# Optimization experiments

Hardware: AMD Instinct MI355X
Metric: run time of the kernel (lower is better)

Reference implementation:

```python
import jax, jax.numpy as jnp
import numpy as np

B, L, DIM, N_STATE, K_CONV = 2, 2048, 1024, 16, 4


def setup_inputs() -> dict:
    key = jax.random.key(0)
    ks = jax.random.split(key, 6)
    sc = lambda k, shape, s: jax.random.normal(k, shape, jnp.float32) * s
    return {
        "x": jax.random.normal(ks[0], (B, L, DIM), jnp.float32),
        "in_proj_w": sc(ks[1], (2 * DIM, DIM), 0.02),
        "conv_w": sc(ks[2], (DIM, 1, K_CONV), 0.1),
        "conv_b": jnp.zeros((DIM,), jnp.float32),
        "x_proj_w": sc(ks[3], (2 * N_STATE + DIM, DIM), 0.02),
        "D_param": jnp.ones((DIM,), jnp.float32),
        "out_proj_w": sc(ks[4], (DIM, DIM), 0.02),
    }


def reference(x, in_proj_w, conv_w, conv_b, x_proj_w, D_param, out_proj_w):
    b, l, d = x.shape
    n = (x_proj_w.shape[0] - d) // 2
    k = conv_w.shape[-1]
    # A buffer: -[1..n] broadcast over channels -> [d, n]
    A = -(jnp.arange(1, n + 1, dtype=x.dtype)[None, :] * jnp.ones((d, 1), x.dtype))

    xz = x @ in_proj_w.T                       # [b, l, 2d]
    x_c, z = xz[..., :d], xz[..., d:]

    # depthwise causal conv (torch pads both sides k-1 then truncates to l == left-pad k-1)
    xc = jnp.transpose(x_c, (0, 2, 1))          # [b, d, l]
    xc = jax.lax.conv_general_dilated(
        xc, conv_w, window_strides=(1,), padding=[(k - 1, 0)],
        dimension_numbers=("NCH", "OIH", "NCH"), feature_group_count=d)
    xc = xc + conv_b[None, :, None]
    xc = jax.nn.silu(jnp.transpose(xc, (0, 2, 1)))  # [b, l, d]

    x_dbl = xc @ x_proj_w.T                    # [b, l, 2n + d]
    B_ssm = x_dbl[..., :n]                     # [b, l, n]
    C_ssm = x_dbl[..., n:2 * n]                # [b, l, n]
    dt = jax.nn.softplus(x_dbl[..., 2 * n:])   # [b, l, d]

    dA = jnp.exp(dt[..., None] * A[None, None])            # [b, l, d, n]
    dBx = (dt[..., None] * B_ssm[:, :, None, :]) * xc[..., None]  # dB * x, [b, l, d, n]

    def step(h, inputs):
        dA_t, dBx_t, C_t = inputs              # [b,d,n], [b,d,n], [b,n]
        h = h * dA_t + dBx_t
        y_t = jnp.einsum("bdn,bn->bd", h, C_t)
        return h, y_t

    h0 = jnp.zeros((b, d, n), x.dtype)
    _, ys = jax.lax.scan(
        step, h0,
        (jnp.moveaxis(dA, 1, 0), jnp.moveaxis(dBx, 1, 0), jnp.moveaxis(C_ssm, 1, 0)))
    y = jnp.moveaxis(ys, 0, 1) + D_param * xc  # [b, l, d]
    y = y * jax.nn.silu(z)
    return y @ out_proj_w.T
```

## Files before the change

kernel.cpp:

```cpp
#include <hip/hip_runtime.h>
#include <cmath>

#define BB   2
#define LL   2048
#define DIMD 1024
#define NS   16
#define KC   4
#define ML   (BB*LL)
#define XZ_N (2*DIMD)
#define XD_N (2*NS + DIMD)
#define LC   16
#define NC   (LL/LC)

typedef __attribute__((ext_vector_type(8))) short bf16x8;
typedef __attribute__((ext_vector_type(4))) float f32x4;

__device__ __forceinline__ unsigned short f2bf(float f) {
    union { float f; unsigned u; } v; v.f = f;
    unsigned r = v.u + 0x7FFF + ((v.u >> 16) & 1);
    return (unsigned short)(r >> 16);
}
__device__ __forceinline__ float bf2f(unsigned short u) {
    union { unsigned u; float f; } v; v.u = (unsigned)u << 16;
    return v.f;
}
__device__ __forceinline__ float silu_f(float a) {
    return a / (1.f + __expf(-a));
}
__device__ __forceinline__ void dt_decay(float raw, float& dt, float& e) {
    const float t = __expf(fminf(raw, 80.f));
    e  = 1.f / (1.f + t);
    dt = (raw > 15.f) ? raw : -__logf(e);
}

__global__ __launch_bounds__(256) void cvt_all(
    const float* __restrict__ s0, unsigned short* __restrict__ d0, int n0,
    const float* __restrict__ s1, unsigned short* __restrict__ d1, int n1,
    const float* __restrict__ s2, unsigned short* __restrict__ d2, int n2,
    const float* __restrict__ s3, unsigned short* __restrict__ d3, int n3)
{
    int i = blockIdx.x * blockDim.x + threadIdx.x;
    const float* src; unsigned short* dst;
    if (i < n0)                { src = s0; dst = d0; }
    else if ((i -= n0) < n1)   { src = s1; dst = d1; }
    else if ((i -= n1) < n2)   { src = s2; dst = d2; }
    else if ((i -= n2) < n3)   { src = s3; dst = d3; }
    else return;
    float4 f = ((const float4*)src)[i];
    ushort4 o;
    o.x = f2bf(f.x); o.y = f2bf(f.y); o.z = f2bf(f.z); o.w = f2bf(f.w);
    ((ushort4*)dst)[i] = o;
}

__global__ __launch_bounds__(256) void gemm_mfma_bt(
    const unsigned short* __restrict__ A,
    const unsigned short* __restrict__ Bw,
    float* __restrict__ C,
    unsigned short* __restrict__ zb,
    int M, int N, int K, int nsplit)
{
    __shared__ short As[2][128 * 64];
    __shared__ short Bs[2][64 * 64];

    const int nwg  = gridDim.x * gridDim.y;
    int wgid = blockIdx.y * gridDim.x + blockIdx.x;
    const int cpx = nwg >> 3;
    wgid = (wgid & 7) * cpx + (wgid >> 3);
    const int bx = wgid % gridDim.x;
    const int by = wgid / gridDim.x;

    const int tid  = threadIdx.x;
    const int lane = tid & 63;
    const int wave = tid >> 6;
    const int bm = by * 128;
    const int bn = bx * 64;
    const int wm = wave * 32;
    const int l15  = lane & 15;
    const int quad = lane >> 4;

    f32x4 acc[2][4];
    #pragma unroll
    for (int i = 0; i < 2; ++i)
        #pragma unroll
        for (int j = 0; j < 4; ++j)
            acc[i][j] = (f32x4){0.f, 0.f, 0.f, 0.f};

    const int NK = K >> 6;

    auto stage = [&](int s, int k0) {
        #pragma unroll
        for (int q = 0; q < 4; ++q) {
            const int ci = q * 256 + tid;
            const int r  = ci >> 3;
            const int cc = (ci & 7) ^ (r & 7);
            short* ldsA = &As[s][0] + (size_t)(q * 256 + (tid & ~63)) * 8;
            const unsigned short* ga = A + (size_t)(bm + r) * K + k0 + cc * 8;
            __builtin_amdgcn_global_load_lds(
                (const __attribute__((address_space(1))) void*)ga,
                (__attribute__((address_space(3))) void*)ldsA, 16, 0, 0);
        }
        #pragma unroll
        for (int q = 0; q < 2; ++q) {
            const int ci = q * 256 + tid;
            const int r  = ci >> 3;
            const int cc = (ci & 7) ^ (r & 7);
            short* ldsB = &Bs[s][0] + (size_t)(q * 256 + (tid & ~63)) * 8;
            int rb = bn + r; if (rb > N - 1) rb = N - 1;
            const unsigned short* gb = Bw + (size_t)rb * K + k0 + cc * 8;
            __builtin_amdgcn_global_load_lds(
                (const __attribute__((address_space(1))) void*)gb,
                (__attribute__((address_space(3))) void*)ldsB, 16, 0, 0);
        }
    };

    stage(0, 0);

    int cur = 0;
    for (int t = 0; t < NK; ++t) {
        if (t + 1 < NK) {
            stage(cur ^ 1, (t + 1) * 64);
            asm volatile("s_waitcnt vmcnt(6)" ::: "memory");
        } else {
            asm volatile("s_waitcnt vmcnt(0)" ::: "memory");
        }
        __builtin_amdgcn_s_barrier();

        const short* Ab = &As[cur][0];
        const short* Bb = &Bs[cur][0];
        #pragma unroll
        for (int kh = 0; kh < 2; ++kh) {
            bf16x8 af[2], bfr[4];
            #pragma unroll
            for (int i = 0; i < 2; ++i) {
                const int row = wm + i * 16 + l15;
                const int pc  = (kh * 4 + quad) ^ (row & 7);
                af[i] = *(const bf16x8*)(Ab + row * 64 + pc * 8);
            }
            #pragma unroll
            for (int j = 0; j < 4; ++j) {
                const int row = j * 16 + l15;
                const int pc  = (kh * 4 + quad) ^ (row & 7);
                bfr[j] = *(const bf16x8*)(Bb + row * 64 + pc * 8);
            }
            #pragma unroll
            for (int i = 0; i < 2; ++i)
                #pragma unroll
                for (int j = 0; j < 4; ++j)
                    acc[i][j] = __builtin_amdgcn_mfma_f32_16x16x32_bf16(
                        af[i], bfr[j], acc[i][j], 0, 0, 0);
        }

        if (t + 1 < NK) __builtin_amdgcn_s_barrier();
        cur ^= 1;
    }

    #pragma unroll
    for (int i = 0; i < 2; ++i) {
        const int rbase = bm + wm + i * 16 + quad * 4;
        #pragma unroll
        for (int j = 0; j < 4; ++j) {
            const int col = bn + j * 16 + l15;
            if (col < nsplit) {
                #pragma unroll
                for (int r = 0; r < 4; ++r)
                    C[(size_t)(rbase + r) * nsplit + col] = acc[i][j][r];
            } else if (col < N) {
                const int zc = col - nsplit;
                #pragma unroll
                for (int r = 0; r < 4; ++r)
                    zb[(size_t)(rbase + r) * DIMD + zc] = f2bf(silu_f(acc[i][j][r]));
            }
        }
    }
}

__global__ __launch_bounds__(256) void conv_silu(const float* __restrict__ xcraw,
                                                 const float* __restrict__ w,
                                                 const float* __restrict__ bias,
                                                 float* __restrict__ xc,
                                                 unsigned short* __restrict__ xcb)
{
    const int i4 = blockIdx.x * blockDim.x + threadIdx.x;
    if (i4 >= ML * DIMD / 4) return;
    const int dq = i4 & (DIMD / 4 - 1);
    const int bl = i4 >> 8;
    const int l  = bl & (LL - 1);

    const float4 wq0 = ((const float4*)w)[dq * 4 + 0];
    const float4 wq1 = ((const float4*)w)[dq * 4 + 1];
    const float4 wq2 = ((const float4*)w)[dq * 4 + 2];
    const float4 wq3 = ((const float4*)w)[dq * 4 + 3];
    const float4 bv  = ((const float4*)bias)[dq];

    const float* p = xcraw + (size_t)bl * DIMD + dq * 4;
    const float4 z4 = make_float4(0.f, 0.f, 0.f, 0.f);
    const float4 x0 = (l >= 3) ? *(const float4*)(p - 3 * DIMD) : z4;
    const float4 x1 = (l >= 2) ? *(const float4*)(p - 2 * DIMD) : z4;
    const float4 x2 = (l >= 1) ? *(const float4*)(p - 1 * DIMD) : z4;
    const float4 x3 = *(const float4*)p;

    float4 a;
    a.x = bv.x + wq0.x*x0.x + wq0.y*x1.x + wq0.z*x2.x + wq0.w*x3.x;
    a.y = bv.y + wq1.x*x0.y + wq1.y*x1.y + wq1.z*x2.y + wq1.w*x3.y;
    a.z = bv.z + wq2.x*x0.z + wq2.y*x1.z + wq2.z*x2.z + wq2.w*x3.z;
    a.w = bv.w + wq3.x*x0.w + wq3.y*x1.w + wq3.z*x2.w + wq3.w*x3.w;

    float4 v;
    v.x = silu_f(a.x); v.y = silu_f(a.y); v.z = silu_f(a.z); v.w = silu_f(a.w);

    ((float4*)xc)[i4] = v;
    ushort4 o;
    o.x = f2bf(v.x); o.y = f2bf(v.y); o.z = f2bf(v.z); o.w = f2bf(v.w);
    ((ushort4*)xcb)[i4] = o;
}

__global__ __launch_bounds__(256) void scan_part1(const float* __restrict__ xdbl,
                                                  const float* __restrict__ xc,
                                                  float* __restrict__ hfin,
                                                  float* __restrict__ Ssum)
{
    __shared__ float Bsh[LC][NS];

    const int tid = threadIdx.x;
    const int idx = blockIdx.x * 256 + tid;
    const int d   = idx & (DIMD - 1);
    const int bc  = idx >> 10;
    const int c   = bc & (NC - 1);
    const int b   = bc >> 7;
    const int l0  = c * LC;

    const float* xdbl_p = xdbl + ((size_t)b * LL + l0) * XD_N;
    const float* xc_p   = xc   + ((size_t)b * LL + l0) * DIMD + d;

    if (tid < LC * NS / 4) {
        const int l = tid >> 2, q = tid & 3;
        ((float4*)&Bsh[l][0])[q] = ((const float4*)(xdbl_p + (size_t)l * XD_N))[q];
    }
    __syncthreads();

    float raw[LC], xcv[LC];
    #pragma unroll
    for (int i = 0; i < LC; ++i) raw[i] = xdbl_p[(size_t)i * XD_N + 2 * NS + d];
    #pragma unroll
    for (int i = 0; i < LC; ++i) xcv[i] = xc_p[(size_t)i * DIMD];

    float e[LC], dx[LC];
    float S = 0.f;
    #pragma unroll
    for (int i = 0; i < LC; ++i) {
        float dt, ev;
        dt_decay(raw[i], dt, ev);
        S += dt;
        e[i]  = ev;
        dx[i] = dt * xcv[i];
    }

    float h[NS];
    #pragma unroll
    for (int n = 0; n < NS; ++n) h[n] = 0.f;

    #pragma unroll
    for (int i = 0; i < LC; ++i) {
        const float4* BC = (const float4*)&Bsh[i][0];
        const float4 B0 = BC[0], B1 = BC[1], B2 = BC[2], B3 = BC[3];
        const float ev = e[i], dxv = dx[i];
        const float e2 = ev * ev, e4 = e2 * e2;
        float p0 = ev, p1 = e2, p2 = e2 * ev, p3 = e4;
        h[0]  = fmaf(h[0],  p0, dxv * B0.x);
        h[1]  = fmaf(h[1],  p1, dxv * B0.y);
        h[2]  = fmaf(h[2],  p2, dxv * B0.z);
        h[3]  = fmaf(h[3],  p3, dxv * B0.w);
        p0 *= e4; p1 *= e4; p2 *= e4; p3 *= e4;
        h[4]  = fmaf(h[4],  p0, dxv * B1.x);
        h[5]  = fmaf(h[5],  p1, dxv * B1.y);
        h[6]  = fmaf(h[6],  p2, dxv * B1.z);
        h[7]  = fmaf(h[7],  p3, dxv * B1.w);
        p0 *= e4; p1 *= e4; p2 *= e4; p3 *= e4;
        h[8]  = fmaf(h[8],  p0, dxv * B2.x);
        h[9]  = fmaf(h[9],  p1, dxv * B2.y);
        h[10] = fmaf(h[10], p2, dxv * B2.z);
        h[11] = fmaf(h[11], p3, dxv * B2.w);
        p0 *= e4; p1 *= e4; p2 *= e4; p3 *= e4;
        h[12] = fmaf(h[12], p0, dxv * B3.x);
        h[13] = fmaf(h[13], p1, dxv * B3.y);
        h[14] = fmaf(h[14], p2, dxv * B3.z);
        h[15] = fmaf(h[15], p3, dxv * B3.w);
    }

    float4* hf = (float4*)(hfin + (size_t)idx * NS);
    #pragma unroll
    for (int n = 0; n < 4; ++n) hf[n] = ((float4*)h)[n];
    Ssum[idx] = S;
}

#define NGRP 8
#define CPG  (NC / NGRP)
__global__ __launch_bounds__(256) void scan_combine(float* __restrict__ hfin,
                                                    const float* __restrict__ Ssum)
{
    __shared__ float Ash[2][NGRP][NS];
    __shared__ float Bsh2[2][NGRP][NS];

    const int tid = threadIdx.x;
    const int n   = tid & (NS - 1);
    const int g   = (tid >> 4) & (NGRP - 1);
    const int d2  = tid >> 7;
    const int bd  = blockIdx.x * 2 + d2;
    const int d   = bd & (DIMD - 1);
    const int b   = bd >> 10;
    const float np1 = (float)(n + 1);
    const int c0 = g * CPG;

    float e[CPG], hb[CPG];
    #pragma unroll
    for (int j = 0; j < CPG; ++j) {
        const size_t base = ((size_t)(b * NC + c0 + j) * DIMD + d);
        const float S = Ssum[base];
        hb[j] = hfin[base * NS + n];
        e[j]  = __expf(-S * np1);
    }

    float A = 1.f, Bv = 0.f;
    #pragma unroll
    for (int j = 0; j < CPG; ++j) { Bv = fmaf(Bv, e[j], hb[j]); A *= e[j]; }

    Ash[d2][g][n] = A;  Bsh2[d2][g][n] = Bv;
    __syncthreads();

    float hc = 0.f;
    for (int j = 0; j < g; ++j) hc = fmaf(hc, Ash[d2][j][n], Bsh2[d2][j][n]);

    #pragma unroll
    for (int j = 0; j < CPG; ++j) {
        const size_t o = ((size_t)(b * NC + c0 + j) * DIMD + d) * NS + n;
        hfin[o] = hc;
        hc = fmaf(hc, e[j], hb[j]);
    }
}

__global__ __launch_bounds__(256) void scan_part2(const float* __restrict__ xdbl,
                                                  const float* __restrict__ xc,
                                                  const unsigned short* __restrict__ zb,
                                                  const float* __restrict__ hfin,
                                                  const float* __restrict__ Dp,
                                                  unsigned short* __restrict__ yout)
{
    __shared__ float BCs[LC][2 * NS];

    const int tid = threadIdx.x;
    const int idx = blockIdx.x * 256 + tid;
    const int d   = idx & (DIMD - 1);
    const int bc  = idx >> 10;
    const int c   = bc & (NC - 1);
    const int b   = bc >> 7;
    const int l0  = c * LC;

    const float* xdbl_p = xdbl + ((size_t)b * LL + l0) * XD_N;
    const float* xc_p   = xc   + ((size_t)b * LL + l0) * DIMD + d;
    const unsigned short* zb_p = zb + ((size_t)b * LL + l0) * DIMD + d;
    unsigned short* y_p = yout + ((size_t)b * LL + l0) * DIMD + d;

    if (tid < LC * 2 * NS / 4) {
        const int l = tid >> 3, q = tid & 7;
        ((float4*)&BCs[l][0])[q] = ((const float4*)(xdbl_p + (size_t)l * XD_N))[q];
    }
    __syncthreads();

    float raw[LC], xcv[LC], zg[LC];
    #pragma unroll
    for (int i = 0; i < LC; ++i) raw[i] = xdbl_p[(size_t)i * XD_N + 2 * NS + d];
    #pragma unroll
    for (int i = 0; i < LC; ++i) xcv[i] = xc_p[(size_t)i * DIMD];
    #pragma unroll
    for (int i = 0; i < LC; ++i) zg[i] = bf2f(zb_p[(size_t)i * DIMD]);

    float e[LC], dx[LC];
    #pragma unroll
    for (int i = 0; i < LC; ++i) {
        float dt, ev;
        dt_decay(raw[i], dt, ev);
        e[i]  = ev;
        dx[i] = dt * xcv[i];
    }

    const float Dv = Dp[d];
    float h[NS];
    {
        const float4* hf = (const float4*)(hfin + (size_t)idx * NS);
        #pragma unroll
        for (int n = 0; n < 4; ++n) ((float4*)h)[n] = hf[n];
    }

    #pragma unroll
    for (int i = 0; i < LC; ++i) {
        const float4* BC = (const float4*)&BCs[i][0];
        const float4 B0 = BC[0], B1 = BC[1], B2 = BC[2], B3 = BC[3];
        const float4 C0 = BC[4], C1 = BC[5], C2 = BC[6], C3 = BC[7];
        const float ev = e[i], dxv = dx[i];
        const float e2 = ev * ev, e4 = e2 * e2;
        float p0 = ev, p1 = e2, p2 = e2 * ev, p3 = e4;
        float y0, y1, y2, y3;
        h[0]  = fmaf(h[0],  p0, dxv * B0.x); y0 = h[0]  * C0.x;
        h[1]  = fmaf(h[1],  p1, dxv * B0.y); y1 = h[1]  * C0.y;
        h[2]  = fmaf(h[2],  p2, dxv * B0.z); y2 = h[2]  * C0.z;
        h[3]  = fmaf(h[3],  p3, dxv * B0.w); y3 = h[3]  * C0.w;
        p0 *= e4; p1 *= e4; p2 *= e4; p3 *= e4;
        h[4]  = fmaf(h[4],  p0, dxv * B1.x); y0 = fmaf(h[4],  C1.x, y0);
        h[5]  = fmaf(h[5],  p1, dxv * B1.y); y1 = fmaf(h[5],  C1.y, y1);
        h[6]  = fmaf(h[6],  p2, dxv * B1.z); y2 = fmaf(h[6],  C1.z, y2);
        h[7]  = fmaf(h[7],  p3, dxv * B1.w); y3 = fmaf(h[7],  C1.w, y3);
        p0 *= e4; p1 *= e4; p2 *= e4; p3 *= e4;
        h[8]  = fmaf(h[8],  p0, dxv * B2.x); y0 = fmaf(h[8],  C2.x, y0);
        h[9]  = fmaf(h[9],  p1, dxv * B2.y); y1 = fmaf(h[9],  C2.y, y1);
        h[10] = fmaf(h[10], p2, dxv * B2.z); y2 = fmaf(h[10], C2.z, y2);
        h[11] = fmaf(h[11], p3, dxv * B2.w); y3 = fmaf(h[11], C2.w, y3);
        p0 *= e4; p1 *= e4; p2 *= e4; p3 *= e4;
        h[12] = fmaf(h[12], p0, dxv * B3.x); y0 = fmaf(h[12], C3.x, y0);
        h[13] = fmaf(h[13], p1, dxv * B3.y); y1 = fmaf(h[13], C3.y, y1);
        h[14] = fmaf(h[14], p2, dxv * B3.z); y2 = fmaf(h[14], C3.z, y2);
        h[15] = fmaf(h[15], p3, dxv * B3.w); y3 = fmaf(h[15], C3.w, y3);

        const float y  = (y0 + y1) + (y2 + y3);
        const float yv = fmaf(Dv, xcv[i], y);
        y_p[(size_t)i * DIMD] = f2bf(yv * zg[i]);
    }
}

extern "C" void kernel_launch(void* const* d_in, const int* in_sizes, int n_in,
                              void* d_out, int out_size, void* d_ws, size_t ws_size,
                              hipStream_t stream)
{
    const float* x          = (const float*)d_in[0];
    const float* in_proj_w  = (const float*)d_in[1];
    const float* conv_w     = (const float*)d_in[2];
    const float* conv_b     = (const float*)d_in[3];
    const float* x_proj_w   = (const float*)d_in[4];
    const float* D_param    = (const float*)d_in[5];
    const float* out_proj_w = (const float*)d_in[6];
    float* out = (float*)d_out;

    float* xcraw = (float*)d_ws;
    float* xc    = xcraw + (size_t)ML * DIMD;
    float* xdbl  = xc    + (size_t)ML * DIMD;
    unsigned short* zb  = (unsigned short*)(xdbl + (size_t)ML * XD_N);
    unsigned short* xb  = zb  + (size_t)ML * DIMD;
    unsigned short* xcb = xb  + (size_t)ML * DIMD;
    unsigned short* wb1 = xcb + (size_t)ML * DIMD;
    unsigned short* wb2 = wb1 + (size_t)XZ_N * DIMD;
    unsigned short* wb3 = wb2 + (size_t)XD_N * DIMD;
    float* hfin = (float*)(wb3 + (size_t)DIMD * DIMD);
    float* Ssum = hfin + (size_t)BB * NC * DIMD * NS;
    unsigned short* yb  = xb;

    const int n0 = ML * DIMD / 4, n1 = XZ_N * DIMD / 4,
              n2 = XD_N * DIMD / 4, n3 = DIMD * DIMD / 4;
    const int ncvt = n0 + n1 + n2 + n3;

    cvt_all<<<(ncvt + 255) / 256, 256, 0, stream>>>(
        x, xb, n0, in_proj_w, wb1, n1, x_proj_w, wb2, n2, out_proj_w, wb3, n3);

    gemm_mfma_bt<<<dim3(XZ_N / 64, ML / 128), 256, 0, stream>>>(
        xb, wb1, xcraw, zb, ML, XZ_N, DIMD, DIMD);

    conv_silu<<<(ML * DIMD / 4) / 256, 256, 0, stream>>>(
        xcraw, conv_w, conv_b, xc, xcb);

    gemm_mfma_bt<<<dim3((XD_N + 63) / 64, ML / 128), 256, 0, stream>>>(
        xcb, wb2, xdbl, nullptr, ML, XD_N, DIMD, XD_N);

    scan_part1<<<(BB * NC * DIMD) / 256, 256, 0, stream>>>(xdbl, xc, hfin, Ssum);
    scan_combine<<<(BB * DIMD) / 2, 256, 0, stream>>>(hfin, Ssum);
    scan_part2<<<(BB * NC * DIMD) / 256, 256, 0, stream>>>(xdbl, xc, zb, hfin,
                                                           D_param, yb);

    gemm_mfma_bt<<<dim3(DIMD / 64, ML / 128), 256, 0, stream>>>(
        yb, wb3, out, nullptr, ML, DIMD, DIMD, DIMD);
}
```

Before: 211.8 us.

## Fuse depthwise causal conv and SiLU into the in_proj GEMM epilogue

The in_proj GEMM now loads 16 extra halo rows of A per tile and computes the preceding rows' x outputs with one extra MFMA per k-step. The epilogue then stages the accumulators in LDS and applies the 4-tap causal conv, bias and SiLU, writing xc in fp32 and bf16 directly. This removes the separate conv_silu kernel and the fp32 xcraw round trip through global memory. In exchange it recomputes halo rows, enlarges LDS use and adds an extra load and MFMA per iteration, plus two barriers in the epilogue.

After: 196.9 us. -7.0%, faster.

```diff
diff --git a/kernel.cpp b/kernel.cpp
--- a/kernel.cpp
+++ b/kernel.cpp
@@ -52,14 +52,20 @@
     ((ushort4*)dst)[i] = o;
 }
 
+template<bool CONV>
 __global__ __launch_bounds__(256) void gemm_mfma_bt(
     const unsigned short* __restrict__ A,
     const unsigned short* __restrict__ Bw,
     float* __restrict__ C,
     unsigned short* __restrict__ zb,
+    const float* __restrict__ cw,
+    const float* __restrict__ cb,
+    float* __restrict__ xcf,
+    unsigned short* __restrict__ xcbo,
     int M, int N, int K, int nsplit)
 {
-    __shared__ short As[2][128 * 64];
+    constexpr int AROWS = CONV ? 144 : 128;
+    __shared__ short As[2][AROWS * 64];
     __shared__ short Bs[2][64 * 64];
 
     const int nwg  = gridDim.x * gridDim.y;
@@ -78,12 +84,15 @@
     const int l15  = lane & 15;
     const int quad = lane >> 4;
 
+    const bool doConv = CONV && (bn < nsplit);
+
     f32x4 acc[2][4];
     #pragma unroll
     for (int i = 0; i < 2; ++i)
         #pragma unroll
         for (int j = 0; j < 4; ++j)
             acc[i][j] = (f32x4){0.f, 0.f, 0.f, 0.f};
+    f32x4 accx = (f32x4){0.f, 0.f, 0.f, 0.f};
 
     const int NK = K >> 6;
 
@@ -91,13 +100,28 @@
         #pragma unroll
         for (int q = 0; q < 4; ++q) {
             const int ci = q * 256 + tid;
-            const int r  = ci >> 3;
-            const int cc = (ci & 7) ^ (r & 7);
+            const int srow = ci >> 3;
+            const int cc = (ci & 7) ^ (srow & 7);
             short* ldsA = &As[s][0] + (size_t)(q * 256 + (tid & ~63)) * 8;
-            const unsigned short* ga = A + (size_t)(bm + r) * K + k0 + cc * 8;
+            int ra = CONV ? (bm - 16 + srow) : (bm + srow);
+            if (CONV && ra < 0) ra = 0;
+            const unsigned short* ga = A + (size_t)ra * K + k0 + cc * 8;
             __builtin_amdgcn_global_load_lds(
                 (const __attribute__((address_space(1))) void*)ga,
                 (__attribute__((address_space(3))) void*)ldsA, 16, 0, 0);
+        }
+        if constexpr (CONV) {
+            if (lane < 32) {
+                const int ci5 = 1024 + wave * 32 + lane;
+                const int srow = ci5 >> 3;
+                const int cc = (ci5 & 7) ^ (srow & 7);
+                short* ldsA = &As[s][0] + (size_t)(1024 + wave * 32) * 8;
+                const unsigned short* ga =
+                    A + (size_t)(bm - 16 + srow) * K + k0 + cc * 8;
+                __builtin_amdgcn_global_load_lds(
+                    (const __attribute__((address_space(1))) void*)ga,
+                    (__attribute__((address_space(3))) void*)ldsA, 16, 0, 0);
+            }
         }
         #pragma unroll
         for (int q = 0; q < 2; ++q) {
@@ -119,7 +143,10 @@
     for (int t = 0; t < NK; ++t) {
         if (t + 1 < NK) {
             stage(cur ^ 1, (t + 1) * 64);
-            asm volatile("s_waitcnt vmcnt(6)" ::: "memory");
+            if constexpr (CONV)
+                asm volatile("s_waitcnt vmcnt(7)" ::: "memory");
+            else
+                asm volatile("s_waitcnt vmcnt(6)" ::: "memory");
         } else {
             asm volatile("s_waitcnt vmcnt(0)" ::: "memory");
         }
@@ -132,9 +159,9 @@
             bf16x8 af[2], bfr[4];
             #pragma unroll
             for (int i = 0; i < 2; ++i) {
-                const int row = wm + i * 16 + l15;
-                const int pc  = (kh * 4 + quad) ^ (row & 7);
-                af[i] = *(const bf16x8*)(Ab + row * 64 + pc * 8);
+                const int srow = (CONV ? 16 : 0) + wm + i * 16 + l15;
+                const int pc  = (kh * 4 + quad) ^ (srow & 7);
+                af[i] = *(const bf16x8*)(Ab + srow * 64 + pc * 8);
             }
             #pragma unroll
             for (int j = 0; j < 4; ++j) {
@@ -148,70 +175,77 @@
                 for (int j = 0; j < 4; ++j)
                     acc[i][j] = __builtin_amdgcn_mfma_f32_16x16x32_bf16(
                         af[i], bfr[j], acc[i][j], 0, 0, 0);
+            if (doConv) {
+                const int pcA = (kh * 4 + quad) ^ (l15 & 7);
+                bf16x8 afx = *(const bf16x8*)(Ab + l15 * 64 + pcA * 8);
+                const int rowB = wave * 16 + l15;
+                const int pcB = (kh * 4 + quad) ^ (rowB & 7);
+                bf16x8 bfx = *(const bf16x8*)(Bb + rowB * 64 + pcB * 8);
+                accx = __builtin_amdgcn_mfma_f32_16x16x32_bf16(
+                    afx, bfx, accx, 0, 0, 0);
+            }
         }
 
         if (t + 1 < NK) __builtin_amdgcn_s_barrier();
         cur ^= 1;
     }
 
-    #pragma unroll
-    for (int i = 0; i < 2; ++i) {
-        const int rbase = bm + wm + i * 16 + quad * 4;
-        #pragma unroll
-        for (int j = 0; j < 4; ++j) {
-            const int col = bn + j * 16 + l15;
-            if (col < nsplit) {
+    if (doConv) {
+        __syncthreads();
+        float* xcs = (float*)&As[0][0];
+        #pragma unroll
+        for (int i = 0; i < 2; ++i)
+            #pragma unroll
+            for (int j = 0; j < 4; ++j)
                 #pragma unroll
                 for (int r = 0; r < 4; ++r)
-                    C[(size_t)(rbase + r) * nsplit + col] = acc[i][j][r];
-            } else if (col < N) {
-                const int zc = col - nsplit;
-                #pragma unroll
-                for (int r = 0; r < 4; ++r)
-                    zb[(size_t)(rbase + r) * DIMD + zc] = f2bf(silu_f(acc[i][j][r]));
+                    xcs[(16 + wm + i * 16 + quad * 4 + r) * 64 + j * 16 + l15]
+                        = acc[i][j][r];
+        #pragma unroll
+        for (int r = 0; r < 4; ++r)
+            xcs[(quad * 4 + r) * 64 + wave * 16 + l15] = accx[r];
+        __syncthreads();
+
+        const int col = tid & 63;
+        const int gc  = bn + col;
+        const float4 wv  = ((const float4*)cw)[gc];
+        const float  bvv = cb[gc];
+        #pragma unroll
+        for (int k = 0; k < 32; ++k) {
+            const int r  = (tid >> 6) + k * 4;
+            const int gr = bm + r;
+            const int l  = gr & (LL - 1);
+            const float xm3 = (l >= 3) ? xcs[(r + 13) * 64 + col] : 0.f;
+            const float xm2 = (l >= 2) ? xcs[(r + 14) * 64 + col] : 0.f;
+            const float xm1 = (l >= 1) ? xcs[(r + 15) * 64 + col] : 0.f;
+            const float xm0 = xcs[(r + 16) * 64 + col];
+            const float a = bvv + wv.x * xm3 + wv.y * xm2
+                                + wv.z * xm1 + wv.w * xm0;
+            const float v = silu_f(a);
+            xcf[(size_t)gr * DIMD + gc]  = v;
+            xcbo[(size_t)gr * DIMD + gc] = f2bf(v);
+        }
+    } else {
+        #pragma unroll
+        for (int i = 0; i < 2; ++i) {
+            const int rbase = bm + wm + i * 16 + quad * 4;
+            #pragma unroll
+            for (int j = 0; j < 4; ++j) {
+                const int colc = bn + j * 16 + l15;
+                if (colc < nsplit) {
+                    #pragma unroll
+                    for (int r = 0; r < 4; ++r)
+                        C[(size_t)(rbase + r) * nsplit + colc] = acc[i][j][r];
+                } else if (colc < N) {
+                    const int zc = colc - nsplit;
+                    #pragma unroll
+                    for (int r = 0; r < 4; ++r)
+                        zb[(size_t)(rbase + r) * DIMD + zc]
+                            = f2bf(silu_f(acc[i][j][r]));
+                }
             }
         }
     }
-}
-
-__global__ __launch_bounds__(256) void conv_silu(const float* __restrict__ xcraw,
-                                                 const float* __restrict__ w,
-                                                 const float* __restrict__ bias,
-                                                 float* __restrict__ xc,
-                                                 unsigned short* __restrict__ xcb)
-{
-    const int i4 = blockIdx.x * blockDim.x + threadIdx.x;
-    if (i4 >= ML * DIMD / 4) return;
-    const int dq = i4 & (DIMD / 4 - 1);
-    const int bl = i4 >> 8;
-    const int l  = bl & (LL - 1);
-
-    const float4 wq0 = ((const float4*)w)[dq * 4 + 0];
-    const float4 wq1 = ((const float4*)w)[dq * 4 + 1];
-    const float4 wq2 = ((const float4*)w)[dq * 4 + 2];
-    const float4 wq3 = ((const float4*)w)[dq * 4 + 3];
-    const float4 bv  = ((const float4*)bias)[dq];
-
-    const float* p = xcraw + (size_t)bl * DIMD + dq * 4;
-    const float4 z4 = make_float4(0.f, 0.f, 0.f, 0.f);
-    const float4 x0 = (l >= 3) ? *(const float4*)(p - 3 * DIMD) : z4;
-    const float4 x1 = (l >= 2) ? *(const float4*)(p - 2 * DIMD) : z4;
-    const float4 x2 = (l >= 1) ? *(const float4*)(p - 1 * DIMD) : z4;
-    const float4 x3 = *(const float4*)p;
-
-    float4 a;
-    a.x = bv.x + wq0.x*x0.x + wq0.y*x1.x + wq0.z*x2.x + wq0.w*x3.x;
-    a.y = bv.y + wq1.x*x0.y + wq1.y*x1.y + wq1.z*x2.y + wq1.w*x3.y;
-    a.z = bv.z + wq2.x*x0.z + wq2.y*x1.z + wq2.z*x2.z + wq2.w*x3.z;
-    a.w = bv.w + wq3.x*x0.w + wq3.y*x1.w + wq3.z*x2.w + wq3.w*x3.w;
-
-    float4 v;
-    v.x = silu_f(a.x); v.y = silu_f(a.y); v.z = silu_f(a.z); v.w = silu_f(a.w);
-
-    ((float4*)xc)[i4] = v;
-    ushort4 o;
-    o.x = f2bf(v.x); o.y = f2bf(v.y); o.z = f2bf(v.z); o.w = f2bf(v.w);
-    ((ushort4*)xcb)[i4] = o;
 }
 
 __global__ __launch_bounds__(256) void scan_part1(const float* __restrict__ xdbl,
@@ -459,20 +493,19 @@
     cvt_all<<<(ncvt + 255) / 256, 256, 0, stream>>>(
         x, xb, n0, in_proj_w, wb1, n1, x_proj_w, wb2, n2, out_proj_w, wb3, n3);
 
-    gemm_mfma_bt<<<dim3(XZ_N / 64, ML / 128), 256, 0, stream>>>(
-        xb, wb1, xcraw, zb, ML, XZ_N, DIMD, DIMD);
-
-    conv_silu<<<(ML * DIMD / 4) / 256, 256, 0, stream>>>(
-        xcraw, conv_w, conv_b, xc, xcb);
-
-    gemm_mfma_bt<<<dim3((XD_N + 63) / 64, ML / 128), 256, 0, stream>>>(
-        xcb, wb2, xdbl, nullptr, ML, XD_N, DIMD, XD_N);
+    gemm_mfma_bt<true><<<dim3(XZ_N / 64, ML / 128), 256, 0, stream>>>(
+        xb, wb1, nullptr, zb, conv_w, conv_b, xc, xcb, ML, XZ_N, DIMD, DIMD);
+
+    gemm_mfma_bt<false><<<dim3((XD_N + 63) / 64, ML / 128), 256, 0, stream>>>(
+        xcb, wb2, xdbl, nullptr, nullptr, nullptr, nullptr, nullptr,
+        ML, XD_N, DIMD, XD_N);
 
     scan_part1<<<(BB * NC * DIMD) / 256, 256, 0, stream>>>(xdbl, xc, hfin, Ssum);
     scan_combine<<<(BB * DIMD) / 2, 256, 0, stream>>>(hfin, Ssum);
     scan_part2<<<(BB * NC * DIMD) / 256, 256, 0, stream>>>(xdbl, xc, zb, hfin,
                                                            D_param, yb);
 
-    gemm_mfma_bt<<<dim3(DIMD / 64, ML / 128), 256, 0, stream>>>(
-        yb, wb3, out, nullptr, ML, DIMD, DIMD, DIMD);
-}
+    gemm_mfma_bt<false><<<dim3(DIMD / 64, ML / 128), 256, 0, stream>>>(
+        yb, wb3, out, nullptr, nullptr, nullptr, nullptr, nullptr,
+        ML, DIMD, DIMD, DIMD);
+}
```
